# Kernel optimization log

Hardware: AMD Instinct MI355X
Metric: run time of the kernel (lower is better)

## Reference

```python
import jax, jax.numpy as jnp
import numpy as np
import math

PHI = (1.0 + math.sqrt(5.0)) / 2.0
TWO_PI = 2.0 * math.pi

V, D, L, N, RES = 50257, 128, 2, 256, 4096
B, S = 2, 512

# global sin/cos lookup tables over [0, 2*pi), matching get_global_lut(lut_resolution)
_grid = jnp.arange(RES, dtype=jnp.float32) * (TWO_PI / RES)
SIN_T = jnp.sin(_grid)
COS_T = jnp.cos(_grid)


def lut_sin_cos(theta):
    # quantize phase to table index (Python-style mod keeps result non-negative)
    idx = jnp.floor(theta * (RES / TWO_PI)).astype(jnp.int32) % RES
    return SIN_T[idx], COS_T[idx]


def setup_inputs() -> dict:
    key = jax.random.key(0)
    ks = jax.random.split(key, 10)
    xav_c = 0.5 * math.sqrt(2.0 / (2 * D + D))   # xavier gain=0.5 for input_collapse
    xav_o = 0.5 * math.sqrt(2.0 / (N + D))       # xavier for out_proj
    xav_v = 0.5 * math.sqrt(2.0 / (D + V))       # xavier for ComplexLinear
    return {
        "input_ids": jax.random.randint(ks[0], (B, S), 0, V),
        "emb": jax.random.normal(ks[1], (V, 2 * D), jnp.float32) * (0.02 * 0.5),
        "cw": jax.random.normal(ks[2], (L, D, 2 * D), jnp.float32) * xav_c,
        "cb": jnp.zeros((L, D), jnp.float32),
        "W": jax.random.normal(ks[3], (L, N, D), jnp.float32) * 0.02,
        "Bp": jnp.zeros((L, N, D), jnp.float32),
        "attn_cos": jnp.ones((L, N, D), jnp.float32),
        "attn_sin": jnp.ones((L, N, D), jnp.float32),
        "opr": jax.random.normal(ks[4], (L, D, N), jnp.float32) * xav_o,
        "opi": jax.random.normal(ks[5], (L, D, N), jnp.float32) * xav_o,
        "Wr": jax.random.normal(ks[6], (V, D), jnp.float32) * xav_v,
        "Wi": jax.random.normal(ks[7], (V, D), jnp.float32) * xav_v,
    }


def reference(input_ids, emb, cw, cb, W, Bp, attn_cos, attn_sin, opr, opi, Wr, Wi):
    e = emb[input_ids]                         # (B,S,2D) token embedding
    xr, xi = e[..., :D], e[..., D:]            # complex hidden state parts
    t = (jnp.arange(S, dtype=jnp.float32) * PHI)[None, :, None, None]  # golden-ratio timesteps
    for l in range(L):
        xc = jnp.concatenate([xr, xi], axis=-1) @ cw[l].T + cb[l]      # (B,S,D) input collapse
        wavelength = 1.0 + jnp.abs(W[l])                               # (N,D)
        theta = xc[:, :, None, :] / wavelength + Bp[l] + t             # (B,S,N,D)
        s, c = lut_sin_cos(theta)
        cos_sum = jnp.einsum('bsnd,nd->bsn', c, attn_cos[l])           # interference sums
        sin_sum = jnp.einsum('bsnd,nd->bsn', s, attn_sin[l])
        xr = jax.nn.silu(cos_sum @ opr[l].T)                           # (B,S,D)
        xi = jax.nn.silu(sin_sum @ opi[l].T)
    # ComplexLinear output projection (no bias), then collapse to real logits via magnitude
    lr = xr @ Wr.T - xi @ Wi.T
    li = xi @ Wr.T + xr @ Wi.T
    return jnp.sqrt(lr * lr + li * li + 1e-8)  # (B,S,V)
```

## Files before the change

kernel.cpp:

```cpp
#include <hip/hip_runtime.h>
#include <math.h>

#define VV 50257
#define Dm 128
#define NN 256
#define RESN 4096
#define SEQ 512
#define TOK 1024

using f32x4_t = __attribute__((ext_vector_type(4))) float;
using s16x8_t = __attribute__((ext_vector_type(8))) short;
using u16x4_t = __attribute__((ext_vector_type(4))) unsigned short;
using i32x4_t = __attribute__((ext_vector_type(4))) int;

static __device__ __forceinline__ unsigned short f2bf(float f) {
    unsigned u = __builtin_bit_cast(unsigned, f);
    u += 0x7fffu + ((u >> 16) & 1u);
    return (unsigned short)(u >> 16);
}

__global__ void pack_kernel(const float* __restrict__ W, const float* __restrict__ Bp,
                            const float* __restrict__ ac, const float* __restrict__ as_,
                            const float* __restrict__ cw, const float* __restrict__ opr,
                            const float* __restrict__ opi,
                            float4* __restrict__ packed, float* __restrict__ cwT,
                            float* __restrict__ oprT, float* __restrict__ opiT,
                            float2* __restrict__ lutg) {
    int tid = blockIdx.x * 256 + threadIdx.x;
    int l = tid >> 15;
    int rem = tid & 32767;
    {
        int d = rem >> 8, n = rem & 255;
        int src = (l * NN + n) * Dm + d;
        float4 pk;
        pk.x = 1.0f / (1.0f + fabsf(W[src]));
        pk.y = Bp[src];
        pk.z = ac[src];
        pk.w = as_[src];
        packed[tid] = pk;
    }
    {
        int k = rem >> 7, d = rem & 127;
        cwT[tid] = cw[(l * Dm + d) * (2 * Dm) + k];
    }
    {
        int n = rem >> 7, d = rem & 127;
        oprT[tid] = opr[(l * Dm + d) * NN + n];
        opiT[tid] = opi[(l * Dm + d) * NN + n];
    }
    if (tid < RESN) {
        float ang = (float)tid * (float)(6.283185307179586476925286766559 / 4096.0);
        lutg[tid] = make_float2(sinf(ang), cosf(ang));
    }
}

__global__ void wconv_kernel(const float* __restrict__ Wr, const float* __restrict__ Wi,
                             unsigned short* __restrict__ Wr_bf,
                             unsigned short* __restrict__ Wi_bf) {
    int gid = blockIdx.x * 256 + threadIdx.x;
    int base = gid * 4;
    if (base < VV * Dm) {
        float4 r = *(const float4*)(Wr + base);
        float4 w = *(const float4*)(Wi + base);
        *(u16x4_t*)(Wr_bf + base) = (u16x4_t){f2bf(r.x), f2bf(r.y), f2bf(r.z), f2bf(r.w)};
        *(u16x4_t*)(Wi_bf + base) = (u16x4_t){f2bf(w.x), f2bf(w.y), f2bf(w.z), f2bf(w.w)};
    }
}

__global__ void embed_kernel(const int* __restrict__ ids, const float* __restrict__ emb,
                             float* __restrict__ x) {
    int t = blockIdx.x;
    int k = threadIdx.x;
    x[t * 256 + k] = emb[(size_t)ids[t] * 256 + k];
}

__global__ void xc_kernel(const float* __restrict__ x, const float* __restrict__ cwT,
                          const float* __restrict__ cb, float* __restrict__ xc, int l) {
    __shared__ float xs[2][256];
    int tid = threadIdx.x;
    int t0 = blockIdx.x * 2;
    xs[0][tid] = x[t0 * 256 + tid];
    xs[1][tid] = x[(t0 + 1) * 256 + tid];
    __syncthreads();
    int j = tid >> 7, d = tid & 127;
    const float* cwb = cwT + l * 32768;
    float acc = 0.f;
#pragma unroll 8
    for (int k = 0; k < 256; k++) acc = fmaf(xs[j][k], cwb[k * 128 + d], acc);
    xc[(t0 + j) * 128 + d] = acc + cb[l * 128 + d];
}

__global__ void __launch_bounds__(256) theta_kernel(const float* __restrict__ xc,
                                                    const float4* __restrict__ packed,
                                                    const float2* __restrict__ lutg,
                                                    float* __restrict__ pr_part,
                                                    float* __restrict__ pi_part, int l) {
    __shared__ float2 lut[RESN];
    __shared__ float xcs[4][64];
    int tid = threadIdx.x;
    int t0 = blockIdx.x * 4;
    int dh = blockIdx.y;
    const float4* lg = (const float4*)lutg;
    float4* ldst = (float4*)lut;
#pragma unroll
    for (int i = 0; i < 8; i++) ldst[tid + i * 256] = lg[tid + i * 256];
    {
        int j = tid >> 6, i = tid & 63;
        xcs[j][i] = xc[(t0 + j) * 128 + dh * 64 + i];
    }
    __syncthreads();
    float tv[4];
#pragma unroll
    for (int j = 0; j < 4; j++) {
        int s = (t0 + j) & (SEQ - 1);
        tv[j] = (float)s * 1.61803398874989485f;
    }
    const float4* pk = packed + ((size_t)(l * Dm + dh * 64)) * NN + tid;
    float cs[4] = {0, 0, 0, 0}, sn[4] = {0, 0, 0, 0};
    const float SC = (float)(4096.0 / 6.283185307179586476925286766559);
    for (int d = 0; d < 64; d++) {
        float4 p = pk[(size_t)d * NN];
#pragma unroll
        for (int j = 0; j < 4; j++) {
            float th = fmaf(xcs[j][d], p.x, p.y) + tv[j];
            int idx = ((int)floorf(th * SC)) & (RESN - 1);
            float2 scv = lut[idx];
            cs[j] = fmaf(scv.y, p.z, cs[j]);
            sn[j] = fmaf(scv.x, p.w, sn[j]);
        }
    }
#pragma unroll
    for (int j = 0; j < 4; j++) {
        pr_part[(size_t)(dh * TOK + t0 + j) * NN + tid] = cs[j];
        pi_part[(size_t)(dh * TOK + t0 + j) * NN + tid] = sn[j];
    }
}

__global__ void proj_kernel(const float* __restrict__ pr_part, const float* __restrict__ pi_part,
                            const float* __restrict__ oprT, const float* __restrict__ opiT,
                            float* __restrict__ x, unsigned short* __restrict__ x_bf, int l) {
    __shared__ float prs[4][256], pis[4][256];
    int tid = threadIdx.x;
    int t0 = blockIdx.x * 4;
#pragma unroll
    for (int i = 0; i < 4; i++) {
        prs[i][tid] = pr_part[(size_t)(t0 + i) * 256 + tid] +
                      pr_part[(size_t)(TOK + t0 + i) * 256 + tid];
        pis[i][tid] = pi_part[(size_t)(t0 + i) * 256 + tid] +
                      pi_part[(size_t)(TOK + t0 + i) * 256 + tid];
    }
    __syncthreads();
    int g = tid >> 7, d = tid & 127;
    const float* wb = (g == 0 ? oprT : opiT) + l * 32768;
    const float(*ps)[256] = (g == 0) ? prs : pis;
    float acc[4] = {0, 0, 0, 0};
    for (int n = 0; n < 256; n++) {
        float wv = wb[n * 128 + d];
#pragma unroll
        for (int j = 0; j < 4; j++) acc[j] = fmaf(ps[j][n], wv, acc[j]);
    }
#pragma unroll
    for (int j = 0; j < 4; j++) {
        float v = acc[j];
        float s = v / (1.0f + expf(-v));
        x[(t0 + j) * 256 + g * 128 + d] = s;
        x_bf[(t0 + j) * 256 + g * 128 + d] = f2bf(s);
    }
}

__global__ void __launch_bounds__(256, 2) final_kernel(const unsigned short* __restrict__ x_bf,
                                                       const unsigned short* __restrict__ Wr_bf,
                                                       const unsigned short* __restrict__ Wi_bf,
                                                       float* __restrict__ out) {
    __shared__ unsigned short As[128 * 72];
    __shared__ unsigned short B1s[128 * 72];
    __shared__ unsigned short B2s[128 * 72];
    int tid = threadIdx.x;
    int wg = blockIdx.x;
    int wgid = (wg & 7) * 393 + (wg >> 3);
    int vb = wgid >> 3, tb = wgid & 7;
    int v0 = vb * 128;
    int t0 = tb * 128;
    int wave = tid >> 6, lane = tid & 63;
    int wm = wave >> 1, wn = wave & 1;
    int quad = lane >> 4, t16 = lane & 15;

    f32x4_t accR[4][4], accI[4][4];
#pragma unroll
    for (int im = 0; im < 4; im++)
#pragma unroll
        for (int in = 0; in < 4; in++) {
            accR[im][in] = (f32x4_t){0.f, 0.f, 0.f, 0.f};
            accI[im][in] = (f32x4_t){0.f, 0.f, 0.f, 0.f};
        }

    const i32x4_t NEG = {(int)0x80008000, (int)0x80008000, (int)0x80008000, (int)0x80008000};

    for (int kc = 0; kc < 4; kc++) {
        __syncthreads();
        int kbase = (kc & 1) * 64;
        const unsigned short* b1src = (kc < 2) ? Wr_bf : Wi_bf;
        const unsigned short* b2src = (kc < 2) ? Wi_bf : Wr_bf;
#pragma unroll
        for (int i = 0; i < 4; i++) {
            int idx = tid + i * 256;
            int row = idx >> 3, c8 = idx & 7;
            i32x4_t a = *(const i32x4_t*)(x_bf + (size_t)(t0 + row) * 256 + kc * 64 + c8 * 8);
            *(i32x4_t*)(As + row * 72 + c8 * 8) = a;
            int v = v0 + row;
            if (v >= VV) v = VV - 1;
            i32x4_t b1 = *(const i32x4_t*)(b1src + (size_t)v * 128 + kbase + c8 * 8);
            i32x4_t b2 = *(const i32x4_t*)(b2src + (size_t)v * 128 + kbase + c8 * 8);
            if (kc >= 2) b1 ^= NEG;
            *(i32x4_t*)(B1s + row * 72 + c8 * 8) = b1;
            *(i32x4_t*)(B2s + row * 72 + c8 * 8) = b2;
        }
        __syncthreads();
#pragma unroll
        for (int ks = 0; ks < 2; ks++) {
            int kofs = ks * 32 + quad * 8;
            s16x8_t af[4], bR[4], bI[4];
#pragma unroll
            for (int im = 0; im < 4; im++)
                af[im] = *(const s16x8_t*)(As + (wm * 64 + im * 16 + t16) * 72 + kofs);
#pragma unroll
            for (int in = 0; in < 4; in++) {
                bR[in] = *(const s16x8_t*)(B1s + (wn * 64 + in * 16 + t16) * 72 + kofs);
                bI[in] = *(const s16x8_t*)(B2s + (wn * 64 + in * 16 + t16) * 72 + kofs);
            }
#pragma unroll
            for (int im = 0; im < 4; im++)
#pragma unroll
                for (int in = 0; in < 4; in++) {
                    accR[im][in] = __builtin_amdgcn_mfma_f32_16x16x32_bf16(
                        af[im], bR[in], accR[im][in], 0, 0, 0);
                    accI[im][in] = __builtin_amdgcn_mfma_f32_16x16x32_bf16(
                        af[im], bI[in], accI[im][in], 0, 0, 0);
                }
        }
    }
#pragma unroll
    for (int im = 0; im < 4; im++) {
        int tbase = t0 + wm * 64 + im * 16 + quad * 4;
#pragma unroll
        for (int in = 0; in < 4; in++) {
            int v = v0 + wn * 64 + in * 16 + t16;
            if (v < VV) {
#pragma unroll
                for (int r = 0; r < 4; r++) {
                    float lr = accR[im][in][r];
                    float li = accI[im][in][r];
                    out[(size_t)(tbase + r) * VV + v] = sqrtf(fmaf(lr, lr, fmaf(li, li, 1e-8f)));
                }
            }
        }
    }
}

extern "C" void kernel_launch(void* const* d_in, const int* in_sizes, int n_in,
                              void* d_out, int out_size, void* d_ws, size_t ws_size,
                              hipStream_t stream) {
    const int* ids   = (const int*)d_in[0];
    const float* emb = (const float*)d_in[1];
    const float* cw  = (const float*)d_in[2];
    const float* cb  = (const float*)d_in[3];
    const float* W   = (const float*)d_in[4];
    const float* Bp  = (const float*)d_in[5];
    const float* ac  = (const float*)d_in[6];
    const float* as_ = (const float*)d_in[7];
    const float* opr = (const float*)d_in[8];
    const float* opi = (const float*)d_in[9];
    const float* Wr  = (const float*)d_in[10];
    const float* Wi  = (const float*)d_in[11];
    float* out = (float*)d_out;

    char* ws = (char*)d_ws;
    float*  x       = (float*)(ws);
    float*  xc      = (float*)(ws + (1u << 20));
    float*  pr_part = (float*)(ws + (2u << 20));
    float*  pi_part = (float*)(ws + (4u << 20));
    float4* packed  = (float4*)(ws + (6u << 20));
    float*  cwT     = (float*)(ws + (7u << 20));
    float*  oprT    = (float*)(ws + (7u << 20) + (256u << 10));
    float*  opiT    = (float*)(ws + (7u << 20) + (512u << 10));
    float2* lutg    = (float2*)(ws + (7u << 20) + (768u << 10));
    unsigned short* x_bf  = (unsigned short*)(ws + (8u  << 20));
    unsigned short* Wr_bf = (unsigned short*)(ws + (9u  << 20));
    unsigned short* Wi_bf = (unsigned short*)(ws + (22u << 20));

    pack_kernel<<<256, 256, 0, stream>>>(W, Bp, ac, as_, cw, opr, opi,
                                         packed, cwT, oprT, opiT, lutg);
    wconv_kernel<<<(VV * Dm / 4 + 255) / 256, 256, 0, stream>>>(Wr, Wi, Wr_bf, Wi_bf);
    embed_kernel<<<TOK, 256, 0, stream>>>(ids, emb, x);
    for (int l = 0; l < 2; l++) {
        xc_kernel<<<TOK / 2, 256, 0, stream>>>(x, cwT, cb, xc, l);
        theta_kernel<<<dim3(TOK / 4, 2), 256, 0, stream>>>(xc, packed, lutg,
                                                           pr_part, pi_part, l);
        proj_kernel<<<TOK / 4, 256, 0, stream>>>(pr_part, pi_part, oprT, opiT, x, x_bf, l);
    }
    final_kernel<<<dim3(8 * 393), 256, 0, stream>>>(x_bf, Wr_bf, Wi_bf, out);
}
```

Measured before the change: 443.7 us.

## Double-buffer final GEMM via direct global-to-LDS loads with four-accumulator complex math

Rewrites the output-projection GEMM so tiles are copied straight from global memory into a swizzled, double-buffered shared-memory area with global_load_lds, and the next k-chunk is prefetched while the current one is multiplied. The complex product is now formed from four separate real/imag accumulators instead of negating Wi on load. The vocab tile shrinks from 128 to 64, doubling the grid. The aim is to hide load latency, drop the register round-trip into shared memory, and avoid bank conflicts. The cost is more accumulator registers and a smaller tile, which lowers reuse of each weight tile.

```diff
diff --git a/kernel.cpp b/kernel.cpp
--- a/kernel.cpp
+++ b/kernel.cpp
@@ -11,12 +11,17 @@
 using f32x4_t = __attribute__((ext_vector_type(4))) float;
 using s16x8_t = __attribute__((ext_vector_type(8))) short;
 using u16x4_t = __attribute__((ext_vector_type(4))) unsigned short;
-using i32x4_t = __attribute__((ext_vector_type(4))) int;
 
 static __device__ __forceinline__ unsigned short f2bf(float f) {
     unsigned u = __builtin_bit_cast(unsigned, f);
     u += 0x7fffu + ((u >> 16) & 1u);
     return (unsigned short)(u >> 16);
+}
+
+static __device__ __forceinline__ void gload16(const unsigned short* g, unsigned short* l) {
+    __builtin_amdgcn_global_load_lds(
+        (const __attribute__((address_space(1))) unsigned int*)g,
+        (__attribute__((address_space(3))) unsigned int*)l, 16, 0, 0);
 }
 
 __global__ void pack_kernel(const float* __restrict__ W, const float* __restrict__ Bp,
@@ -172,85 +177,105 @@
                                                        const unsigned short* __restrict__ Wr_bf,
                                                        const unsigned short* __restrict__ Wi_bf,
                                                        float* __restrict__ out) {
-    __shared__ unsigned short As[128 * 72];
-    __shared__ unsigned short B1s[128 * 72];
-    __shared__ unsigned short B2s[128 * 72];
+    __shared__ unsigned short lds[2][12288];
     int tid = threadIdx.x;
     int wg = blockIdx.x;
-    int wgid = (wg & 7) * 393 + (wg >> 3);
-    int vb = wgid >> 3, tb = wgid & 7;
-    int v0 = vb * 128;
-    int t0 = tb * 128;
-    int wave = tid >> 6, lane = tid & 63;
-    int wm = wave >> 1, wn = wave & 1;
+    int wp = (wg & 7) * 786 + (wg >> 3);
+    int vb = wp >> 3, tb = wp & 7;
+    int v0 = vb * 64, t0 = tb * 128;
+
+    int wv = tid >> 6, lane = tid & 63;
+    int wm = wv >> 1, wn = wv & 1;
     int quad = lane >> 4, t16 = lane & 15;
 
-    f32x4_t accR[4][4], accI[4][4];
+    int r_loc = lane >> 2;
+    int csw = (lane & 3) ^ ((lane >> 3) & 3);
+    const unsigned short* srcA0 = x_bf + (size_t)(t0 + 32 * wv + r_loc) * 256 + csw * 8;
+    const unsigned short* srcA1 = srcA0 + 16 * 256;
+    int vv_ = v0 + 16 * wv + r_loc;
+    if (vv_ > VV - 1) vv_ = VV - 1;
+    const unsigned short* srcWr = Wr_bf + (size_t)vv_ * 128 + csw * 8;
+    const unsigned short* srcWi = Wi_bf + (size_t)vv_ * 128 + csw * 8;
+
+    int rsw = (t16 >> 1) & 3;
+    int rdA = (wm * 64 + t16) * 32 + ((quad ^ rsw) << 3);
+    int rdB = (wn * 32 + t16) * 32 + ((quad ^ rsw) << 3);
+
+    f32x4_t aRR[4][2], aII[4][2], aIR[4][2], aRI[4][2];
 #pragma unroll
     for (int im = 0; im < 4; im++)
 #pragma unroll
-        for (int in = 0; in < 4; in++) {
-            accR[im][in] = (f32x4_t){0.f, 0.f, 0.f, 0.f};
-            accI[im][in] = (f32x4_t){0.f, 0.f, 0.f, 0.f};
-        }
-
-    const i32x4_t NEG = {(int)0x80008000, (int)0x80008000, (int)0x80008000, (int)0x80008000};
-
+        for (int in = 0; in < 2; in++) {
+            aRR[im][in] = (f32x4_t){0.f, 0.f, 0.f, 0.f};
+            aII[im][in] = (f32x4_t){0.f, 0.f, 0.f, 0.f};
+            aIR[im][in] = (f32x4_t){0.f, 0.f, 0.f, 0.f};
+            aRI[im][in] = (f32x4_t){0.f, 0.f, 0.f, 0.f};
+        }
+
+#define STAGE(b, kc)                                                             \
+    {                                                                            \
+        const int ko = (kc) * 32;                                                \
+        unsigned short* bb = lds[(b)];                                           \
+        gload16(srcA0 + ko, bb + wv * 1024);                                     \
+        gload16(srcA1 + ko, bb + wv * 1024 + 512);                               \
+        gload16(srcA0 + 128 + ko, bb + 4096 + wv * 1024);                        \
+        gload16(srcA1 + 128 + ko, bb + 4096 + wv * 1024 + 512);                  \
+        gload16(srcWr + ko, bb + 8192 + wv * 512);                               \
+        gload16(srcWi + ko, bb + 10240 + wv * 512);                              \
+    }
+
+    STAGE(0, 0);
+#pragma unroll
     for (int kc = 0; kc < 4; kc++) {
-        __syncthreads();
-        int kbase = (kc & 1) * 64;
-        const unsigned short* b1src = (kc < 2) ? Wr_bf : Wi_bf;
-        const unsigned short* b2src = (kc < 2) ? Wi_bf : Wr_bf;
-#pragma unroll
-        for (int i = 0; i < 4; i++) {
-            int idx = tid + i * 256;
-            int row = idx >> 3, c8 = idx & 7;
-            i32x4_t a = *(const i32x4_t*)(x_bf + (size_t)(t0 + row) * 256 + kc * 64 + c8 * 8);
-            *(i32x4_t*)(As + row * 72 + c8 * 8) = a;
-            int v = v0 + row;
-            if (v >= VV) v = VV - 1;
-            i32x4_t b1 = *(const i32x4_t*)(b1src + (size_t)v * 128 + kbase + c8 * 8);
-            i32x4_t b2 = *(const i32x4_t*)(b2src + (size_t)v * 128 + kbase + c8 * 8);
-            if (kc >= 2) b1 ^= NEG;
-            *(i32x4_t*)(B1s + row * 72 + c8 * 8) = b1;
-            *(i32x4_t*)(B2s + row * 72 + c8 * 8) = b2;
-        }
-        __syncthreads();
-#pragma unroll
-        for (int ks = 0; ks < 2; ks++) {
-            int kofs = ks * 32 + quad * 8;
-            s16x8_t af[4], bR[4], bI[4];
-#pragma unroll
-            for (int im = 0; im < 4; im++)
-                af[im] = *(const s16x8_t*)(As + (wm * 64 + im * 16 + t16) * 72 + kofs);
-#pragma unroll
-            for (int in = 0; in < 4; in++) {
-                bR[in] = *(const s16x8_t*)(B1s + (wn * 64 + in * 16 + t16) * 72 + kofs);
-                bI[in] = *(const s16x8_t*)(B2s + (wn * 64 + in * 16 + t16) * 72 + kofs);
+        if (kc < 3) {
+            STAGE((kc + 1) & 1, kc + 1);
+            asm volatile("s_waitcnt vmcnt(6)" ::: "memory");
+        } else {
+            asm volatile("s_waitcnt vmcnt(0)" ::: "memory");
+        }
+        __builtin_amdgcn_s_barrier();
+        __builtin_amdgcn_sched_barrier(0);
+        const unsigned short* B = lds[kc & 1];
+        s16x8_t ar[4], ai[4], fr[2], fi[2];
+#pragma unroll
+        for (int im = 0; im < 4; im++) {
+            ar[im] = *(const s16x8_t*)(B + rdA + im * 512);
+            ai[im] = *(const s16x8_t*)(B + 4096 + rdA + im * 512);
+        }
+#pragma unroll
+        for (int in = 0; in < 2; in++) {
+            fr[in] = *(const s16x8_t*)(B + 8192 + rdB + in * 512);
+            fi[in] = *(const s16x8_t*)(B + 10240 + rdB + in * 512);
+        }
+#pragma unroll
+        for (int im = 0; im < 4; im++)
+#pragma unroll
+            for (int in = 0; in < 2; in++) {
+                aRR[im][in] = __builtin_amdgcn_mfma_f32_16x16x32_bf16(ar[im], fr[in],
+                                                                      aRR[im][in], 0, 0, 0);
+                aII[im][in] = __builtin_amdgcn_mfma_f32_16x16x32_bf16(ai[im], fi[in],
+                                                                      aII[im][in], 0, 0, 0);
+                aIR[im][in] = __builtin_amdgcn_mfma_f32_16x16x32_bf16(ai[im], fr[in],
+                                                                      aIR[im][in], 0, 0, 0);
+                aRI[im][in] = __builtin_amdgcn_mfma_f32_16x16x32_bf16(ar[im], fi[in],
+                                                                      aRI[im][in], 0, 0, 0);
             }
-#pragma unroll
-            for (int im = 0; im < 4; im++)
-#pragma unroll
-                for (int in = 0; in < 4; in++) {
-                    accR[im][in] = __builtin_amdgcn_mfma_f32_16x16x32_bf16(
-                        af[im], bR[in], accR[im][in], 0, 0, 0);
-                    accI[im][in] = __builtin_amdgcn_mfma_f32_16x16x32_bf16(
-                        af[im], bI[in], accI[im][in], 0, 0, 0);
-                }
-        }
-    }
+        __builtin_amdgcn_s_barrier();
+    }
+#undef STAGE
+
 #pragma unroll
     for (int im = 0; im < 4; im++) {
-        int tbase = t0 + wm * 64 + im * 16 + quad * 4;
-#pragma unroll
-        for (int in = 0; in < 4; in++) {
-            int v = v0 + wn * 64 + in * 16 + t16;
+        int trow = t0 + wm * 64 + im * 16 + quad * 4;
+#pragma unroll
+        for (int in = 0; in < 2; in++) {
+            int v = v0 + wn * 32 + in * 16 + t16;
             if (v < VV) {
 #pragma unroll
                 for (int r = 0; r < 4; r++) {
-                    float lr = accR[im][in][r];
-                    float li = accI[im][in][r];
-                    out[(size_t)(tbase + r) * VV + v] = sqrtf(fmaf(lr, lr, fmaf(li, li, 1e-8f)));
+                    float lr = aRR[im][in][r] - aII[im][in][r];
+                    float li = aIR[im][in][r] + aRI[im][in][r];
+                    out[(size_t)(trow + r) * VV + v] = sqrtf(fmaf(lr, lr, fmaf(li, li, 1e-8f)));
                 }
             }
         }
@@ -298,5 +323,5 @@
                                                            pr_part, pi_part, l);
         proj_kernel<<<TOK / 4, 256, 0, stream>>>(pr_part, pi_part, oprT, opiT, x, x_bf, l);
     }
-    final_kernel<<<dim3(8 * 393), 256, 0, stream>>>(x_bf, Wr_bf, Wi_bf, out);
-}
+    final_kernel<<<dim3(786 * 8), 256, 0, stream>>>(x_bf, Wr_bf, Wi_bf, out);
+}
```

Result: faster. 431.1 us (-2.8%).
